# Performance work log

Measured on AMD Instinct MI355X. Metric: run time of the kernel, lower is better.

The kernel has to match this reference:

```python
import jax, jax.numpy as jnp
import numpy as np
from jax import lax

C = 64        # channels / number of Phi heads
HID = 8       # Phi hidden size
FEAT = 2 * 8 * 8  # flattened size after conv+pool
EPS = 1e-5
NEG_SLOPE = 0.01


def setup_inputs() -> dict:
    key = jax.random.key(0)
    ks = jax.random.split(key, 12)
    B = 2048
    x1 = jax.random.normal(ks[0], (B, C, 19, 19), dtype=jnp.float32)
    x2 = jax.random.normal(ks[1], (B, C, 19, 19), dtype=jnp.float32)
    s = 0.1
    conv_w = jax.random.normal(ks[2], (C, 2, 2, 3, 3), dtype=jnp.float32) * s
    conv_b = jax.random.normal(ks[3], (C, 2), dtype=jnp.float32) * s
    bn_g = jnp.ones((C, 2), dtype=jnp.float32)
    bn_b = jnp.zeros((C, 2), dtype=jnp.float32)
    fc1_w = jax.random.normal(ks[4], (C, HID, FEAT), dtype=jnp.float32) * s
    fc1_b = jax.random.normal(ks[5], (C, HID), dtype=jnp.float32) * s
    fc2_w = jax.random.normal(ks[6], (C, 1, HID), dtype=jnp.float32) * s
    fc2_b = jax.random.normal(ks[7], (C, 1), dtype=jnp.float32) * s
    w_out = jax.random.normal(ks[8], (1, C), dtype=jnp.float32) * s
    b_out = jax.random.normal(ks[9], (1,), dtype=jnp.float32) * s
    return {
        "x1": x1, "x2": x2,
        "conv_w": conv_w, "conv_b": conv_b,
        "bn_g": bn_g, "bn_b": bn_b,
        "fc1_w": fc1_w, "fc1_b": fc1_b,
        "fc2_w": fc2_w, "fc2_b": fc2_b,
        "w_out": w_out, "b_out": b_out,
    }


def _phi(x, cw, cb, g, b, w1, b1, w2, b2):
    # x: [B,2,19,19], cw: [2,2,3,3]
    y = lax.conv_general_dilated(x, cw, (1, 1), 'VALID',
                                 dimension_numbers=('NCHW', 'OIHW', 'NCHW'))
    y = y + cb[None, :, None, None]                       # [B,2,17,17]
    # BatchNorm2d in training mode: biased batch stats over (N,H,W)
    mean = jnp.mean(y, axis=(0, 2, 3), keepdims=True)
    var = jnp.mean((y - mean) ** 2, axis=(0, 2, 3), keepdims=True)
    y = (y - mean) * lax.rsqrt(var + EPS)
    y = y * g[None, :, None, None] + b[None, :, None, None]
    # LeakyReLU (default slope 0.01)
    y = jnp.where(y > 0, y, NEG_SLOPE * y)
    # MaxPool2d(2): 17x17 -> 8x8 (floor)
    y = lax.reduce_window(y, -jnp.inf, lax.max,
                          (1, 1, 2, 2), (1, 1, 2, 2), 'VALID')
    y = y.reshape(y.shape[0], -1)                         # [B,128]
    y = y @ w1.T + b1                                     # [B,HID]
    y = y @ w2.T + b2                                     # [B,1]
    return y


def reference(x1, x2, conv_w, conv_b, bn_g, bn_b, fc1_w, fc1_b, fc2_w, fc2_b,
              w_out, b_out):
    B = x1.shape[0]
    # per-channel pair input: [C, B, 2, H, W]
    xin = jnp.stack([x1, x2], axis=2).transpose(1, 0, 2, 3, 4)
    outs = jax.vmap(_phi)(xin, conv_w, conv_b, bn_g, bn_b,
                          fc1_w, fc1_b, fc2_w, fc2_b)      # [C, B, 1]
    feat = outs[..., 0].T                                  # [B, C]
    logits = feat @ w_out.T + b_out                        # [B, 1]
    return jax.nn.sigmoid(logits)
```

## Files before the change

### kernel.cpp

```cpp
#include <hip/hip_runtime.h>
#include <math.h>

#define CC    64
#define BATCH 2048
#define EPS   1e-5f
#define SLOPE 0.01f

#define WS_SUMR  0
#define WS_SQR   4096
#define WS_A     8192
#define WS_B     8320
#define WS_WF    8448
#define WS_WB    16640
#define WS_LOGIT 16704
#define WS_POOL  18944
#define WS_NEEDED_BYTES ((size_t)(WS_POOL + (size_t)BATCH * CC * 128) * 4)

__device__ inline unsigned bf16rne(float x) {
    unsigned u = __float_as_uint(x);
    return (u + 0x7fffu + ((u >> 16) & 1u)) >> 16;
}

__device__ inline void pkfma(float2& acc, float2 a, float2 b) {
    asm("v_pk_fma_f32 %0, %1, %2, %0" : "+v"(acc) : "v"(a), "v"(b));
}

template<bool STORE>
__global__ __launch_bounds__(128, 4) void pass1_kernel(
    const float* __restrict__ x1, const float* __restrict__ x2,
    const float* __restrict__ conv_w, const float* __restrict__ conv_b,
    float* __restrict__ ws)
{
    __shared__ __align__(16) float lds[2][2][760];

    int blk = blockIdx.x;
    int tt  = threadIdx.x;
    int wv  = tt >> 6;
    int t   = tt & 63;
    int b     = blk >> 4;
    int cpair = (blk & 15) * 2 + wv;
    int c0    = cpair * 2;

    float (*L)[760] = lds[wv];

    const float2* g1 = (const float2*)(x1 + ((size_t)b * 64 + c0) * 361);
    const float2* g2 = (const float2*)(x2 + ((size_t)b * 64 + c0) * 361);
    #pragma unroll
    for (int sl = 0; sl < 6; sl++) {
        int g = t + 64 * sl;
        if (sl < 5 || g < 361) {
            float2 v1 = g1[g];
            float2 v2 = g2[g];
            unsigned e  = 2u * g;
            unsigned r0 = (e * 110377u) >> 21;
            unsigned r1 = ((e + 1u) * 110377u) >> 21;
            int i0 = e + r0;
            int i1 = e + 1 + r1;
            L[0][i0] = v1.x; L[0][i1] = v1.y;
            L[1][i0] = v2.x; L[1][i1] = v2.y;
        }
    }

    int img = t >> 5;
    int u   = t & 31;
    int o   = u >> 4;
    int p   = u & 15;
    int pi  = p >> 1;
    int pjp = p & 1;
    int c   = c0 + img;

    const float2* wp2 = (const float2*)(conv_w + (size_t)(c * 2 + o) * 18);
    float2 wgt[18];
    #pragma unroll
    for (int j = 0; j < 9; j++) {
        float2 pr = wp2[j];
        wgt[2 * j]     = make_float2(pr.x, pr.x);
        wgt[2 * j + 1] = make_float2(pr.y, pr.y);
    }
    float cbv = conv_b[c * 2 + o];

    __syncthreads();

    float2 A[2][4];
    #pragma unroll
    for (int di = 0; di < 2; di++)
        #pragma unroll
        for (int k = 0; k < 4; k++)
            A[di][k] = make_float2(cbv, cbv);

    int wb = img * 380 + pi * 40 + pjp * 8;

    #pragma unroll
    for (int ic = 0; ic < 2; ic++) {
        const float* plane = &L[ic][wb];
        const float2* wic = &wgt[ic * 9];
        #pragma unroll
        for (int r = 0; r < 4; r++) {
            const float* row = plane + 20 * r;
            float4 a4 = *(const float4*)(row);
            float4 b4 = *(const float4*)(row + 4);
            float2 c2 = *(const float2*)(row + 8);
            float2 P[9];
            P[0] = make_float2(a4.x, a4.y);
            P[1] = make_float2(a4.y, a4.z);
            P[2] = make_float2(a4.z, a4.w);
            P[3] = make_float2(a4.w, b4.x);
            P[4] = make_float2(b4.x, b4.y);
            P[5] = make_float2(b4.y, b4.z);
            P[6] = make_float2(b4.z, b4.w);
            P[7] = make_float2(b4.w, c2.x);
            P[8] = make_float2(c2.x, c2.y);
            #pragma unroll
            for (int di = 0; di < 2; di++) {
                int ki = r - di;
                if (ki < 0 || ki > 2) continue;
                #pragma unroll
                for (int k = 0; k < 4; k++)
                    #pragma unroll
                    for (int kj = 0; kj < 3; kj++)
                        pkfma(A[di][k], P[2 * k + kj], wic[3 * ki + kj]);
            }
        }
    }

    const float2 one2 = make_float2(1.f, 1.f);
    float2 sp = make_float2(0.f, 0.f), q2 = make_float2(0.f, 0.f);
    #pragma unroll
    for (int di = 0; di < 2; di++)
        #pragma unroll
        for (int k = 0; k < 4; k++) {
            pkfma(sp, A[di][k], one2);
            pkfma(q2, A[di][k], A[di][k]);
        }
    float s = sp.x + sp.y;
    float q = q2.x + q2.y;

    if (STORE) {
        unsigned pk[4];
        #pragma unroll
        for (int k = 0; k < 4; k++) {
            float mx = fmaxf(fmaxf(A[0][k].x, A[0][k].y), fmaxf(A[1][k].x, A[1][k].y));
            float mn = fminf(fminf(A[0][k].x, A[0][k].y), fminf(A[1][k].x, A[1][k].y));
            pk[k] = (bf16rne(mx) << 16) | bf16rne(mn);
        }
        uint4* pool4 = (uint4*)(ws + WS_POOL);
        pool4[((size_t)(b * 64 + c)) * 32 + o * 16 + pi * 2 + pjp] =
            make_uint4(pk[0], pk[1], pk[2], pk[3]);
    }

    int ibase = img * 380;
    #pragma unroll
    for (int rep = 0; rep < 2; rep++) {
        int bidx = p + 16 * rep;
        int bi = bidx < 17 ? 16 : bidx - 17;
        int bj = bidx < 17 ? bidx : 16;
        int bw = ibase + 20 * bi + bj;
        float accb = cbv;
        #pragma unroll
        for (int ic = 0; ic < 2; ic++)
            #pragma unroll
            for (int ki = 0; ki < 3; ki++)
                #pragma unroll
                for (int kj = 0; kj < 3; kj++)
                    accb = fmaf(L[ic][bw + 20 * ki + kj], wgt[ic * 9 + ki * 3 + kj].x, accb);
        s += accb; q = fmaf(accb, accb, q);
    }
    if (p == 0) {
        int bw = ibase + 20 * 15 + 16;
        float accb = cbv;
        #pragma unroll
        for (int ic = 0; ic < 2; ic++)
            #pragma unroll
            for (int ki = 0; ki < 3; ki++)
                #pragma unroll
                for (int kj = 0; kj < 3; kj++)
                    accb = fmaf(L[ic][bw + 20 * ki + kj], wgt[ic * 9 + ki * 3 + kj].x, accb);
        s += accb; q = fmaf(accb, accb, q);
    }

    #pragma unroll
    for (int off = 8; off > 0; off >>= 1) {
        s += __shfl_down(s, off, 16);
        q += __shfl_down(q, off, 16);
    }
    if (p == 0) {
        int rep = b & 31;
        atomicAdd(&ws[WS_SUMR + rep * 128 + c * 2 + o], s);
        atomicAdd(&ws[WS_SQR  + rep * 128 + c * 2 + o], q);
    }
}

__global__ __launch_bounds__(128) void prep_kernel(
    const float* __restrict__ bn_g, const float* __restrict__ bn_b,
    const float* __restrict__ fc1_w, const float* __restrict__ fc1_b,
    const float* __restrict__ fc2_w, const float* __restrict__ fc2_b,
    const float* __restrict__ w_out,
    float* __restrict__ ws)
{
    int c = blockIdx.x;
    int f = threadIdx.x;

    float wsum = 0.f;
    #pragma unroll
    for (int h = 0; h < 8; h++)
        wsum += fc2_w[c * 8 + h] * fc1_w[(c * 8 + h) * 128 + f];
    ws[WS_WF + c * 128 + f] = w_out[c] * wsum;

    if (f == 0) {
        float bsum = fc2_b[c];
        #pragma unroll
        for (int h = 0; h < 8; h++)
            bsum += fc2_w[c * 8 + h] * fc1_b[c * 8 + h];
        ws[WS_WB + c] = w_out[c] * bsum;
    }
    if (f < 2) {
        int idx = c * 2 + f;
        float s = 0.f, q = 0.f;
        for (int r = 0; r < 32; r++) {
            s += ws[WS_SUMR + r * 128 + idx];
            q += ws[WS_SQR  + r * 128 + idx];
        }
        const float N = 2048.0f * 289.0f;
        float mean = s / N;
        float var  = q / N - mean * mean;
        float inv  = rsqrtf(var + EPS);
        float A    = bn_g[idx] * inv;
        ws[WS_A + idx] = A;
        ws[WS_B + idx] = bn_b[idx] - mean * A;
    }
}

__global__ __launch_bounds__(256) void pass2_kernel(
    const float* __restrict__ ws, const float* __restrict__ b_out,
    float* __restrict__ out)
{
    __shared__ float red[4];
    int b = blockIdx.x;
    int t = threadIdx.x;
    const uint4* pool = (const uint4*)(ws + WS_POOL) + (size_t)b * 2048;

    float partial = (t < 64) ? ws[WS_WB + t] : 0.f;
    if (t == 0) partial += b_out[0];

    #pragma unroll
    for (int i = 0; i < 8; i++) {
        uint4 p = pool[t + i * 256];
        int k0 = (t + i * 256) * 4;
        float A  = ws[WS_A + (k0 >> 6)];
        float Bs = ws[WS_B + (k0 >> 6)];
        const float4 wf = *(const float4*)&ws[WS_WF + k0];
        unsigned uu[4] = { p.x, p.y, p.z, p.w };
        float wfv[4] = { wf.x, wf.y, wf.z, wf.w };
        #pragma unroll
        for (int j = 0; j < 4; j++) {
            float mx = __uint_as_float(uu[j] & 0xffff0000u);
            float mn = __uint_as_float(uu[j] << 16);
            float val = A > 0.f ? mx : mn;
            float v = fmaf(A, val, Bs);
            v = v > 0.f ? v : SLOPE * v;
            partial = fmaf(v, wfv[j], partial);
        }
    }

    #pragma unroll
    for (int off = 32; off > 0; off >>= 1)
        partial += __shfl_down(partial, off);
    if ((t & 63) == 0) red[t >> 6] = partial;
    __syncthreads();
    if (t == 0) {
        float lsum = red[0] + red[1] + red[2] + red[3];
        out[b] = 1.f / (1.f + expf(-lsum));
    }
}

__global__ __launch_bounds__(128) void main_fb_kernel(
    const float* __restrict__ x1, const float* __restrict__ x2,
    const float* __restrict__ conv_w, const float* __restrict__ conv_b,
    float* __restrict__ ws)
{
    __shared__ float lds[2][19 * 20];
    __shared__ float red[2];

    int blk = blockIdx.x;
    int c = blk & 63;
    int b = blk >> 6;
    int t = threadIdx.x;

    const float* src1 = x1 + (size_t)blk * 361;
    const float* src2 = x2 + (size_t)blk * 361;
    for (int i = t; i < 361; i += 128) {
        int r = i / 19;
        int col = i - r * 19;
        lds[0][r * 20 + col] = src1[i];
        lds[1][r * 20 + col] = src2[i];
    }

    int o = t >> 6;
    int l = t & 63;
    int pi = l >> 3, pj = l & 7;

    const float* wcp = conv_w + c * 36 + o * 18;
    float w0[9], w1[9];
    #pragma unroll
    for (int k = 0; k < 9; k++) { w0[k] = wcp[k]; w1[k] = wcp[9 + k]; }
    float cbv = conv_b[c * 2 + o];
    float A   = ws[WS_A + c * 2 + o];
    float Bs  = ws[WS_B + c * 2 + o];
    float wf  = ws[WS_WF + c * 128 + t];

    __syncthreads();

    float xw[2][4][4];
    int base = (2 * pi) * 20 + 2 * pj;
    #pragma unroll
    for (int ic = 0; ic < 2; ic++)
        #pragma unroll
        for (int r = 0; r < 4; r++)
            #pragma unroll
            for (int cc = 0; cc < 4; cc++)
                xw[ic][r][cc] = lds[ic][base + r * 20 + cc];

    float m = -3.4e38f;
    #pragma unroll
    for (int di = 0; di < 2; di++)
        #pragma unroll
        for (int dj = 0; dj < 2; dj++) {
            float acc = cbv;
            #pragma unroll
            for (int ki = 0; ki < 3; ki++)
                #pragma unroll
                for (int kj = 0; kj < 3; kj++) {
                    acc = fmaf(xw[0][di + ki][dj + kj], w0[ki * 3 + kj], acc);
                    acc = fmaf(xw[1][di + ki][dj + kj], w1[ki * 3 + kj], acc);
                }
            float v = fmaf(A, acc, Bs);
            v = v > 0.f ? v : SLOPE * v;
            m = fmaxf(m, v);
        }

    float contrib = m * wf;
    #pragma unroll
    for (int off = 32; off > 0; off >>= 1)
        contrib += __shfl_down(contrib, off);
    if (l == 0) red[o] = contrib;
    __syncthreads();
    if (t == 0)
        atomicAdd(&ws[WS_LOGIT + b], red[0] + red[1]);
}

__global__ __launch_bounds__(256) void final_fb_kernel(
    const float* __restrict__ ws, const float* __restrict__ b_out,
    float* __restrict__ out)
{
    int b = blockIdx.x * blockDim.x + threadIdx.x;
    if (b >= BATCH) return;
    float bias = b_out[0];
    #pragma unroll
    for (int c = 0; c < CC; c++) bias += ws[WS_WB + c];
    float l = ws[WS_LOGIT + b] + bias;
    out[b] = 1.f / (1.f + expf(-l));
}

extern "C" void kernel_launch(void* const* d_in, const int* in_sizes, int n_in,
                              void* d_out, int out_size, void* d_ws, size_t ws_size,
                              hipStream_t stream) {
    const float* x1     = (const float*)d_in[0];
    const float* x2     = (const float*)d_in[1];
    const float* conv_w = (const float*)d_in[2];
    const float* conv_b = (const float*)d_in[3];
    const float* bn_g   = (const float*)d_in[4];
    const float* bn_b   = (const float*)d_in[5];
    const float* fc1_w  = (const float*)d_in[6];
    const float* fc1_b  = (const float*)d_in[7];
    const float* fc2_w  = (const float*)d_in[8];
    const float* fc2_b  = (const float*)d_in[9];
    const float* w_out  = (const float*)d_in[10];
    const float* b_out  = (const float*)d_in[11];
    float* ws  = (float*)d_ws;
    float* out = (float*)d_out;

    dim3 big(BATCH * 16);
    bool pool_path = ws_size >= WS_NEEDED_BYTES;

    if (pool_path) {
        hipMemsetAsync(d_ws, 0, 8192 * sizeof(float), stream);
        pass1_kernel<true><<<big, 128, 0, stream>>>(x1, x2, conv_w, conv_b, ws);
        prep_kernel<<<CC, 128, 0, stream>>>(bn_g, bn_b, fc1_w, fc1_b, fc2_w, fc2_b, w_out, ws);
        pass2_kernel<<<BATCH, 256, 0, stream>>>(ws, b_out, out);
    } else {
        hipMemsetAsync(d_ws, 0, 18752 * sizeof(float), stream);
        pass1_kernel<false><<<big, 128, 0, stream>>>(x1, x2, conv_w, conv_b, ws);
        prep_kernel<<<CC, 128, 0, stream>>>(bn_g, bn_b, fc1_w, fc1_b, fc2_w, fc2_b, w_out, ws);
        main_fb_kernel<<<dim3(BATCH * CC), 128, 0, stream>>>(x1, x2, conv_w, conv_b, ws);
        final_fb_kernel<<<(BATCH + 255) / 256, 256, 0, stream>>>(ws, b_out, out);
    }
}
```

Baseline: 113.9 us.

## Read conv inputs directly from global memory, dropping LDS staging in pass1

The first pass no longer stages each image pair into shared memory with a padded layout. Each thread now loads its conv window rows straight from global memory with unaligned vector loads. The border outputs (last column and last row) are folded into the main loop and a row-7 branch instead of a separate LDS-based loop. Weights are kept unduplicated and selected via op_sel on packed FMA, and blocks grow to 256 threads covering 8 channel pairs. This removes LDS writes and the barrier, at the cost of overlapping, unaligned global reads that rely on cache and some divergence in the edge branch.

```diff
diff --git a/kernel.cpp b/kernel.cpp
--- a/kernel.cpp
+++ b/kernel.cpp
@@ -16,6 +16,9 @@
 #define WS_POOL  18944
 #define WS_NEEDED_BYTES ((size_t)(WS_POOL + (size_t)BATCH * CC * 128) * 4)
 
+typedef float f4v __attribute__((ext_vector_type(4), aligned(4)));
+typedef float f2v __attribute__((ext_vector_type(2), aligned(4)));
+
 __device__ inline unsigned bf16rne(float x) {
     unsigned u = __float_as_uint(x);
     return (u + 0x7fffu + ((u >> 16) & 1u)) >> 16;
@@ -24,42 +27,31 @@
 __device__ inline void pkfma(float2& acc, float2 a, float2 b) {
     asm("v_pk_fma_f32 %0, %1, %2, %0" : "+v"(acc) : "v"(a), "v"(b));
 }
+__device__ inline void pkfma_l(float2& acc, float2 a, float2 w) {
+    asm("v_pk_fma_f32 %0, %1, %2, %0 op_sel:[0,0,0] op_sel_hi:[1,0,1]"
+        : "+v"(acc) : "v"(a), "v"(w));
+}
+__device__ inline void pkfma_h(float2& acc, float2 a, float2 w) {
+    asm("v_pk_fma_f32 %0, %1, %2, %0 op_sel:[0,1,0] op_sel_hi:[1,1,1]"
+        : "+v"(acc) : "v"(a), "v"(w));
+}
+
+#define WFMA(ACC, XP, FF)                                              \
+    do { if (((FF) & 1) == 0) pkfma_l(ACC, XP, wgt[(FF) >> 1]);        \
+         else                 pkfma_h(ACC, XP, wgt[(FF) >> 1]); } while (0)
+#define WSC(FF) (((FF) & 1) ? wgt[(FF) >> 1].y : wgt[(FF) >> 1].x)
 
 template<bool STORE>
-__global__ __launch_bounds__(128, 4) void pass1_kernel(
+__global__ __launch_bounds__(256, 4) void pass1_kernel(
     const float* __restrict__ x1, const float* __restrict__ x2,
     const float* __restrict__ conv_w, const float* __restrict__ conv_b,
     float* __restrict__ ws)
 {
-    __shared__ __align__(16) float lds[2][2][760];
-
-    int blk = blockIdx.x;
     int tt  = threadIdx.x;
     int wv  = tt >> 6;
     int t   = tt & 63;
-    int b     = blk >> 4;
-    int cpair = (blk & 15) * 2 + wv;
-    int c0    = cpair * 2;
-
-    float (*L)[760] = lds[wv];
-
-    const float2* g1 = (const float2*)(x1 + ((size_t)b * 64 + c0) * 361);
-    const float2* g2 = (const float2*)(x2 + ((size_t)b * 64 + c0) * 361);
-    #pragma unroll
-    for (int sl = 0; sl < 6; sl++) {
-        int g = t + 64 * sl;
-        if (sl < 5 || g < 361) {
-            float2 v1 = g1[g];
-            float2 v2 = g2[g];
-            unsigned e  = 2u * g;
-            unsigned r0 = (e * 110377u) >> 21;
-            unsigned r1 = ((e + 1u) * 110377u) >> 21;
-            int i0 = e + r0;
-            int i1 = e + 1 + r1;
-            L[0][i0] = v1.x; L[0][i1] = v1.y;
-            L[1][i0] = v2.x; L[1][i1] = v2.y;
-        }
-    }
+    int blk = blockIdx.x;
+    int b   = blk >> 3;
 
     int img = t >> 5;
     int u   = t & 31;
@@ -67,19 +59,19 @@
     int p   = u & 15;
     int pi  = p >> 1;
     int pjp = p & 1;
-    int c   = c0 + img;
+    int cpair = (blk & 7) * 4 + wv;
+    int c   = cpair * 2 + img;
+
+    size_t ibase = (size_t)(b * 64 + c) * 361;
+    int wb = 2 * pi * 19 + 8 * pjp;
+    const float* p1 = x1 + ibase + wb;
+    const float* p2 = x2 + ibase + wb;
 
     const float2* wp2 = (const float2*)(conv_w + (size_t)(c * 2 + o) * 18);
-    float2 wgt[18];
-    #pragma unroll
-    for (int j = 0; j < 9; j++) {
-        float2 pr = wp2[j];
-        wgt[2 * j]     = make_float2(pr.x, pr.x);
-        wgt[2 * j + 1] = make_float2(pr.y, pr.y);
-    }
+    float2 wgt[9];
+    #pragma unroll
+    for (int j = 0; j < 9; j++) wgt[j] = wp2[j];
     float cbv = conv_b[c * 2 + o];
-
-    __syncthreads();
 
     float2 A[2][4];
     #pragma unroll
@@ -87,19 +79,17 @@
         #pragma unroll
         for (int k = 0; k < 4; k++)
             A[di][k] = make_float2(cbv, cbv);
-
-    int wb = img * 380 + pi * 40 + pjp * 8;
+    float y16[2] = { cbv, cbv };
 
     #pragma unroll
     for (int ic = 0; ic < 2; ic++) {
-        const float* plane = &L[ic][wb];
-        const float2* wic = &wgt[ic * 9];
+        const float* src = ic ? p2 : p1;
         #pragma unroll
         for (int r = 0; r < 4; r++) {
-            const float* row = plane + 20 * r;
-            float4 a4 = *(const float4*)(row);
-            float4 b4 = *(const float4*)(row + 4);
-            float2 c2 = *(const float2*)(row + 8);
+            const float* row = src + 19 * r;
+            f4v a4 = *(const f4v*)(row);
+            f4v b4 = *(const f4v*)(row + 4);
+            f4v c4 = *(const f4v*)(row + 8);
             float2 P[9];
             P[0] = make_float2(a4.x, a4.y);
             P[1] = make_float2(a4.y, a4.z);
@@ -108,32 +98,101 @@
             P[4] = make_float2(b4.x, b4.y);
             P[5] = make_float2(b4.y, b4.z);
             P[6] = make_float2(b4.z, b4.w);
-            P[7] = make_float2(b4.w, c2.x);
-            P[8] = make_float2(c2.x, c2.y);
+            P[7] = make_float2(b4.w, c4.x);
+            P[8] = make_float2(c4.x, c4.y);
             #pragma unroll
             for (int di = 0; di < 2; di++) {
-                int ki = r - di;
+                const int ki = r - di;
                 if (ki < 0 || ki > 2) continue;
                 #pragma unroll
                 for (int k = 0; k < 4; k++)
                     #pragma unroll
-                    for (int kj = 0; kj < 3; kj++)
-                        pkfma(A[di][k], P[2 * k + kj], wic[3 * ki + kj]);
+                    for (int kj = 0; kj < 3; kj++) {
+                        const int ff = ic * 9 + ki * 3 + kj;
+                        WFMA(A[di][k], P[2 * k + kj], ff);
+                    }
+                {
+                    const int f0 = ic * 9 + ki * 3;
+                    y16[di] = fmaf(c4.x, WSC(f0 + 0), y16[di]);
+                    y16[di] = fmaf(c4.y, WSC(f0 + 1), y16[di]);
+                    y16[di] = fmaf(c4.z, WSC(f0 + 2), y16[di]);
+                }
             }
         }
     }
 
     const float2 one2 = make_float2(1.f, 1.f);
-    float2 sp = make_float2(0.f, 0.f), q2 = make_float2(0.f, 0.f);
+    float2 sp = make_float2(0.f, 0.f), sq = make_float2(0.f, 0.f);
     #pragma unroll
     for (int di = 0; di < 2; di++)
         #pragma unroll
         for (int k = 0; k < 4; k++) {
             pkfma(sp, A[di][k], one2);
-            pkfma(q2, A[di][k], A[di][k]);
+            pkfma(sq, A[di][k], A[di][k]);
         }
     float s = sp.x + sp.y;
-    float q = q2.x + q2.y;
+    float q = sq.x + sq.y;
+
+    if (pjp == 1) {
+        s += y16[0] + y16[1];
+        q = fmaf(y16[0], y16[0], fmaf(y16[1], y16[1], q));
+    }
+
+    if (pi == 7) {
+        float2 Y[4];
+        #pragma unroll
+        for (int j = 0; j < 4; j++) Y[j] = make_float2(cbv, cbv);
+        float yc = cbv;
+        #pragma unroll
+        for (int ic = 0; ic < 2; ic++) {
+            const float* src = ic ? p2 : p1;
+            #pragma unroll
+            for (int ki = 0; ki < 3; ki++) {
+                const float* row = src + 38 + 19 * ki;
+                float xx[11];
+                if (ki < 2) {
+                    f4v a4 = *(const f4v*)(row);
+                    f4v b4 = *(const f4v*)(row + 4);
+                    f4v c4 = *(const f4v*)(row + 8);
+                    xx[0]=a4.x; xx[1]=a4.y; xx[2]=a4.z; xx[3]=a4.w;
+                    xx[4]=b4.x; xx[5]=b4.y; xx[6]=b4.z; xx[7]=b4.w;
+                    xx[8]=c4.x; xx[9]=c4.y; xx[10]=c4.z;
+                } else {
+                    f4v a4 = *(const f4v*)(row);
+                    f4v b4 = *(const f4v*)(row + 4);
+                    f2v d2 = *(const f2v*)(row + 8);
+                    float e1 = row[10];
+                    xx[0]=a4.x; xx[1]=a4.y; xx[2]=a4.z; xx[3]=a4.w;
+                    xx[4]=b4.x; xx[5]=b4.y; xx[6]=b4.z; xx[7]=b4.w;
+                    xx[8]=d2.x; xx[9]=d2.y; xx[10]=e1;
+                }
+                #pragma unroll
+                for (int j = 0; j < 4; j++)
+                    #pragma unroll
+                    for (int kj = 0; kj < 3; kj++) {
+                        const int ff = ic * 9 + ki * 3 + kj;
+                        float2 xp = make_float2(xx[2 * j + kj], xx[2 * j + kj + 1]);
+                        WFMA(Y[j], xp, ff);
+                    }
+                {
+                    const int f0 = ic * 9 + ki * 3;
+                    yc = fmaf(xx[8],  WSC(f0 + 0), yc);
+                    yc = fmaf(xx[9],  WSC(f0 + 1), yc);
+                    yc = fmaf(xx[10], WSC(f0 + 2), yc);
+                }
+            }
+        }
+        float2 sp2 = make_float2(0.f, 0.f), sq2 = make_float2(0.f, 0.f);
+        #pragma unroll
+        for (int j = 0; j < 4; j++) {
+            pkfma(sp2, Y[j], one2);
+            pkfma(sq2, Y[j], Y[j]);
+        }
+        float se = sp2.x + sp2.y;
+        float qe = sq2.x + sq2.y;
+        if (pjp == 1) { se += yc; qe = fmaf(yc, yc, qe); }
+        s += se; q += qe;
+    }
 
     if (STORE) {
         unsigned pk[4];
@@ -146,36 +205,6 @@
         uint4* pool4 = (uint4*)(ws + WS_POOL);
         pool4[((size_t)(b * 64 + c)) * 32 + o * 16 + pi * 2 + pjp] =
             make_uint4(pk[0], pk[1], pk[2], pk[3]);
-    }
-
-    int ibase = img * 380;
-    #pragma unroll
-    for (int rep = 0; rep < 2; rep++) {
-        int bidx = p + 16 * rep;
-        int bi = bidx < 17 ? 16 : bidx - 17;
-        int bj = bidx < 17 ? bidx : 16;
-        int bw = ibase + 20 * bi + bj;
-        float accb = cbv;
-        #pragma unroll
-        for (int ic = 0; ic < 2; ic++)
-            #pragma unroll
-            for (int ki = 0; ki < 3; ki++)
-                #pragma unroll
-                for (int kj = 0; kj < 3; kj++)
-                    accb = fmaf(L[ic][bw + 20 * ki + kj], wgt[ic * 9 + ki * 3 + kj].x, accb);
-        s += accb; q = fmaf(accb, accb, q);
-    }
-    if (p == 0) {
-        int bw = ibase + 20 * 15 + 16;
-        float accb = cbv;
-        #pragma unroll
-        for (int ic = 0; ic < 2; ic++)
-            #pragma unroll
-            for (int ki = 0; ki < 3; ki++)
-                #pragma unroll
-                for (int kj = 0; kj < 3; kj++)
-                    accb = fmaf(L[ic][bw + 20 * ki + kj], wgt[ic * 9 + ki * 3 + kj].x, accb);
-        s += accb; q = fmaf(accb, accb, q);
     }
 
     #pragma unroll
@@ -379,17 +408,16 @@
     float* ws  = (float*)d_ws;
     float* out = (float*)d_out;
 
-    dim3 big(BATCH * 16);
     bool pool_path = ws_size >= WS_NEEDED_BYTES;
 
     if (pool_path) {
         hipMemsetAsync(d_ws, 0, 8192 * sizeof(float), stream);
-        pass1_kernel<true><<<big, 128, 0, stream>>>(x1, x2, conv_w, conv_b, ws);
+        pass1_kernel<true><<<dim3(BATCH * 8), 256, 0, stream>>>(x1, x2, conv_w, conv_b, ws);
         prep_kernel<<<CC, 128, 0, stream>>>(bn_g, bn_b, fc1_w, fc1_b, fc2_w, fc2_b, w_out, ws);
         pass2_kernel<<<BATCH, 256, 0, stream>>>(ws, b_out, out);
     } else {
         hipMemsetAsync(d_ws, 0, 18752 * sizeof(float), stream);
-        pass1_kernel<false><<<big, 128, 0, stream>>>(x1, x2, conv_w, conv_b, ws);
+        pass1_kernel<false><<<dim3(BATCH * 8), 256, 0, stream>>>(x1, x2, conv_w, conv_b, ws);
         prep_kernel<<<CC, 128, 0, stream>>>(bn_g, bn_b, fc1_w, fc1_b, fc2_w, fc2_b, w_out, ws);
         main_fb_kernel<<<dim3(BATCH * CC), 128, 0, stream>>>(x1, x2, conv_w, conv_b, ws);
         final_fb_kernel<<<(BATCH + 255) / 256, 256, 0, stream>>>(ws, b_out, out);
```

After: 172.0 us. 51.1% more time.

## Pack both conv output channels into packed FMA lanes via op_sel broadcast

Applied to the files above, without the earlier changes.

Remaps pass1 threads so each lane computes both output channels for a 2x4 window strip. The two output channels sit in the two halves of a packed v_pk_fma_f32, and op_sel/op_sel_hi select the input scalar, so the old duplicated-weight float2 and the 9 shuffled P pairs go away. This cuts LDS loads and register shuffles per FMA, and the pool store and reduction change to match (32-lane shuffle, two atomics per lane). The inline asm op_sel semantics must be exactly right, and the pool layout changes, which the consumer kernel has to match.

```diff
diff --git a/kernel.cpp b/kernel.cpp
--- a/kernel.cpp
+++ b/kernel.cpp
@@ -23,6 +23,14 @@
 
 __device__ inline void pkfma(float2& acc, float2 a, float2 b) {
     asm("v_pk_fma_f32 %0, %1, %2, %0" : "+v"(acc) : "v"(a), "v"(b));
+}
+__device__ inline void pk_xl(float2& acc, float2 x, float2 w) {
+    asm("v_pk_fma_f32 %0, %1, %2, %0 op_sel:[0,0,0] op_sel_hi:[0,1,1]"
+        : "+v"(acc) : "v"(x), "v"(w));
+}
+__device__ inline void pk_xh(float2& acc, float2 x, float2 w) {
+    asm("v_pk_fma_f32 %0, %1, %2, %0 op_sel:[1,0,0] op_sel_hi:[1,1,1]"
+        : "+v"(acc) : "v"(x), "v"(w));
 }
 
 template<bool STORE>
@@ -62,131 +70,146 @@
     }
 
     int img = t >> 5;
-    int u   = t & 31;
-    int o   = u >> 4;
-    int p   = u & 15;
-    int pi  = p >> 1;
-    int pjp = p & 1;
+    int p   = t & 31;
+    int pi  = p >> 2;
+    int h   = p & 3;
     int c   = c0 + img;
 
-    const float2* wp2 = (const float2*)(conv_w + (size_t)(c * 2 + o) * 18);
-    float2 wgt[18];
+    const float2* wpa = (const float2*)(conv_w + (size_t)(c * 2 + 0) * 18);
+    const float2* wpb = (const float2*)(conv_w + (size_t)(c * 2 + 1) * 18);
+    float2 w2[18];
     #pragma unroll
     for (int j = 0; j < 9; j++) {
-        float2 pr = wp2[j];
-        wgt[2 * j]     = make_float2(pr.x, pr.x);
-        wgt[2 * j + 1] = make_float2(pr.y, pr.y);
-    }
-    float cbv = conv_b[c * 2 + o];
+        float2 pa = wpa[j], pb = wpb[j];
+        w2[2 * j]     = make_float2(pa.x, pb.x);
+        w2[2 * j + 1] = make_float2(pa.y, pb.y);
+    }
+    float2 cb2 = *(const float2*)(conv_b + c * 2);
 
     __syncthreads();
 
-    float2 A[2][4];
+    float2 A2[2][4];
     #pragma unroll
     for (int di = 0; di < 2; di++)
         #pragma unroll
-        for (int k = 0; k < 4; k++)
-            A[di][k] = make_float2(cbv, cbv);
-
-    int wb = img * 380 + pi * 40 + pjp * 8;
+        for (int j = 0; j < 4; j++)
+            A2[di][j] = cb2;
+
+    int wb = img * 380 + pi * 40 + h * 4;
 
     #pragma unroll
     for (int ic = 0; ic < 2; ic++) {
         const float* plane = &L[ic][wb];
-        const float2* wic = &wgt[ic * 9];
         #pragma unroll
         for (int r = 0; r < 4; r++) {
             const float* row = plane + 20 * r;
-            float4 a4 = *(const float4*)(row);
-            float4 b4 = *(const float4*)(row + 4);
-            float2 c2 = *(const float2*)(row + 8);
-            float2 P[9];
-            P[0] = make_float2(a4.x, a4.y);
-            P[1] = make_float2(a4.y, a4.z);
-            P[2] = make_float2(a4.z, a4.w);
-            P[3] = make_float2(a4.w, b4.x);
-            P[4] = make_float2(b4.x, b4.y);
-            P[5] = make_float2(b4.y, b4.z);
-            P[6] = make_float2(b4.z, b4.w);
-            P[7] = make_float2(b4.w, c2.x);
-            P[8] = make_float2(c2.x, c2.y);
+            float4 a4 = *(const float4*)row;
+            float2 d2 = *(const float2*)(row + 4);
+            float2 PA = make_float2(a4.x, a4.y);
+            float2 PB = make_float2(a4.z, a4.w);
+            float2 PC = d2;
             #pragma unroll
             for (int di = 0; di < 2; di++) {
-                int ki = r - di;
+                const int ki = r - di;
                 if (ki < 0 || ki > 2) continue;
-                #pragma unroll
-                for (int k = 0; k < 4; k++)
-                    #pragma unroll
-                    for (int kj = 0; kj < 3; kj++)
-                        pkfma(A[di][k], P[2 * k + kj], wic[3 * ki + kj]);
+                const int f0 = ic * 9 + ki * 3;
+                pk_xl(A2[di][0], PA, w2[f0 + 0]);
+                pk_xh(A2[di][0], PA, w2[f0 + 1]);
+                pk_xl(A2[di][0], PB, w2[f0 + 2]);
+                pk_xh(A2[di][1], PA, w2[f0 + 0]);
+                pk_xl(A2[di][1], PB, w2[f0 + 1]);
+                pk_xh(A2[di][1], PB, w2[f0 + 2]);
+                pk_xl(A2[di][2], PB, w2[f0 + 0]);
+                pk_xh(A2[di][2], PB, w2[f0 + 1]);
+                pk_xl(A2[di][2], PC, w2[f0 + 2]);
+                pk_xh(A2[di][3], PB, w2[f0 + 0]);
+                pk_xl(A2[di][3], PC, w2[f0 + 1]);
+                pk_xh(A2[di][3], PC, w2[f0 + 2]);
             }
         }
     }
 
     const float2 one2 = make_float2(1.f, 1.f);
-    float2 sp = make_float2(0.f, 0.f), q2 = make_float2(0.f, 0.f);
+    float2 sum2 = make_float2(0.f, 0.f), sq2 = make_float2(0.f, 0.f);
     #pragma unroll
     for (int di = 0; di < 2; di++)
         #pragma unroll
-        for (int k = 0; k < 4; k++) {
-            pkfma(sp, A[di][k], one2);
-            pkfma(q2, A[di][k], A[di][k]);
-        }
-    float s = sp.x + sp.y;
-    float q = q2.x + q2.y;
-
-    if (STORE) {
-        unsigned pk[4];
-        #pragma unroll
-        for (int k = 0; k < 4; k++) {
-            float mx = fmaxf(fmaxf(A[0][k].x, A[0][k].y), fmaxf(A[1][k].x, A[1][k].y));
-            float mn = fminf(fminf(A[0][k].x, A[0][k].y), fminf(A[1][k].x, A[1][k].y));
-            pk[k] = (bf16rne(mx) << 16) | bf16rne(mn);
-        }
-        uint4* pool4 = (uint4*)(ws + WS_POOL);
-        pool4[((size_t)(b * 64 + c)) * 32 + o * 16 + pi * 2 + pjp] =
-            make_uint4(pk[0], pk[1], pk[2], pk[3]);
-    }
-
-    int ibase = img * 380;
-    #pragma unroll
-    for (int rep = 0; rep < 2; rep++) {
-        int bidx = p + 16 * rep;
-        int bi = bidx < 17 ? 16 : bidx - 17;
-        int bj = bidx < 17 ? bidx : 16;
-        int bw = ibase + 20 * bi + bj;
-        float accb = cbv;
+        for (int j = 0; j < 4; j++) {
+            pkfma(sum2, A2[di][j], one2);
+            pkfma(sq2, A2[di][j], A2[di][j]);
+        }
+    float s0 = sum2.x, s1 = sum2.y, q0 = sq2.x, q1 = sq2.y;
+
+    {
+        int bi = p < 17 ? 16 : p - 17;
+        int bj = p < 17 ? p  : 16;
+        int bw = img * 380 + bi * 20 + bj;
+        float y0 = cb2.x, y1 = cb2.y;
         #pragma unroll
         for (int ic = 0; ic < 2; ic++)
             #pragma unroll
             for (int ki = 0; ki < 3; ki++)
                 #pragma unroll
-                for (int kj = 0; kj < 3; kj++)
-                    accb = fmaf(L[ic][bw + 20 * ki + kj], wgt[ic * 9 + ki * 3 + kj].x, accb);
-        s += accb; q = fmaf(accb, accb, q);
+                for (int kj = 0; kj < 3; kj++) {
+                    float v = L[ic][bw + 20 * ki + kj];
+                    const int ff = ic * 9 + ki * 3 + kj;
+                    y0 = fmaf(v, w2[ff].x, y0);
+                    y1 = fmaf(v, w2[ff].y, y1);
+                }
+        s0 += y0; q0 = fmaf(y0, y0, q0);
+        s1 += y1; q1 = fmaf(y1, y1, q1);
     }
     if (p == 0) {
-        int bw = ibase + 20 * 15 + 16;
-        float accb = cbv;
+        int bw = img * 380 + 15 * 20 + 16;
+        float y0 = cb2.x, y1 = cb2.y;
         #pragma unroll
         for (int ic = 0; ic < 2; ic++)
             #pragma unroll
             for (int ki = 0; ki < 3; ki++)
                 #pragma unroll
-                for (int kj = 0; kj < 3; kj++)
-                    accb = fmaf(L[ic][bw + 20 * ki + kj], wgt[ic * 9 + ki * 3 + kj].x, accb);
-        s += accb; q = fmaf(accb, accb, q);
-    }
-
-    #pragma unroll
-    for (int off = 8; off > 0; off >>= 1) {
-        s += __shfl_down(s, off, 16);
-        q += __shfl_down(q, off, 16);
+                for (int kj = 0; kj < 3; kj++) {
+                    float v = L[ic][bw + 20 * ki + kj];
+                    const int ff = ic * 9 + ki * 3 + kj;
+                    y0 = fmaf(v, w2[ff].x, y0);
+                    y1 = fmaf(v, w2[ff].y, y1);
+                }
+        s0 += y0; q0 = fmaf(y0, y0, q0);
+        s1 += y1; q1 = fmaf(y1, y1, q1);
+    }
+
+    if (STORE) {
+        float mxA0 = fmaxf(fmaxf(A2[0][0].x, A2[0][1].x), fmaxf(A2[1][0].x, A2[1][1].x));
+        float mnA0 = fminf(fminf(A2[0][0].x, A2[0][1].x), fminf(A2[1][0].x, A2[1][1].x));
+        float mxB0 = fmaxf(fmaxf(A2[0][2].x, A2[0][3].x), fmaxf(A2[1][2].x, A2[1][3].x));
+        float mnB0 = fminf(fminf(A2[0][2].x, A2[0][3].x), fminf(A2[1][2].x, A2[1][3].x));
+        float mxA1 = fmaxf(fmaxf(A2[0][0].y, A2[0][1].y), fmaxf(A2[1][0].y, A2[1][1].y));
+        float mnA1 = fminf(fminf(A2[0][0].y, A2[0][1].y), fminf(A2[1][0].y, A2[1][1].y));
+        float mxB1 = fmaxf(fmaxf(A2[0][2].y, A2[0][3].y), fmaxf(A2[1][2].y, A2[1][3].y));
+        float mnB1 = fminf(fminf(A2[0][2].y, A2[0][3].y), fminf(A2[1][2].y, A2[1][3].y));
+        unsigned* pool = (unsigned*)(ws + WS_POOL);
+        size_t base = ((size_t)(b * 64 + c)) * 128;
+        int cell = pi * 8 + 2 * h;
+        *(uint2*)&pool[base + cell] =
+            make_uint2((bf16rne(mxA0) << 16) | bf16rne(mnA0),
+                       (bf16rne(mxB0) << 16) | bf16rne(mnB0));
+        *(uint2*)&pool[base + 64 + cell] =
+            make_uint2((bf16rne(mxA1) << 16) | bf16rne(mnA1),
+                       (bf16rne(mxB1) << 16) | bf16rne(mnB1));
+    }
+
+    #pragma unroll
+    for (int off = 16; off > 0; off >>= 1) {
+        s0 += __shfl_down(s0, off, 32);
+        q0 += __shfl_down(q0, off, 32);
+        s1 += __shfl_down(s1, off, 32);
+        q1 += __shfl_down(q1, off, 32);
     }
     if (p == 0) {
         int rep = b & 31;
-        atomicAdd(&ws[WS_SUMR + rep * 128 + c * 2 + o], s);
-        atomicAdd(&ws[WS_SQR  + rep * 128 + c * 2 + o], q);
+        atomicAdd(&ws[WS_SUMR + rep * 128 + c * 2 + 0], s0);
+        atomicAdd(&ws[WS_SQR  + rep * 128 + c * 2 + 0], q0);
+        atomicAdd(&ws[WS_SUMR + rep * 128 + c * 2 + 1], s1);
+        atomicAdd(&ws[WS_SQR  + rep * 128 + c * 2 + 1], q1);
     }
 }
 
```

Measured after the change: 115.8 us. Within noise of the previous version (+1.7%).
